# Performance work log

Measured on AMD Instinct MI355X. Metric: run time of the kernel, lower is better.

## Reference

```python
import jax, jax.numpy as jnp
import numpy as np

N_NODES = 50000
N_EDGES = 1_600_000
IN_F, HID, OUT = 256, 256, 64


def setup_inputs() -> dict:
    key = jax.random.key(0)
    ks = jax.random.split(key, 12)
    inp = {
        "x": jax.random.normal(ks[0], (N_NODES, IN_F), dtype=jnp.float32),
        "src": jax.random.randint(ks[1], (N_EDGES,), 0, N_NODES, dtype=jnp.int32),
        "dst": jax.random.randint(ks[2], (N_EDGES,), 0, N_NODES, dtype=jnp.int32),
        "W_self0": jax.random.normal(ks[3], (IN_F, HID), jnp.float32) * (1.0 / np.sqrt(IN_F)),
        "W_neigh0": jax.random.normal(ks[4], (IN_F, HID), jnp.float32) * (1.0 / np.sqrt(IN_F)),
        "b0": jnp.zeros((HID,), jnp.float32),
        "W_self1": jax.random.normal(ks[5], (HID, HID), jnp.float32) * (1.0 / np.sqrt(HID)),
        "W_neigh1": jax.random.normal(ks[6], (HID, HID), jnp.float32) * (1.0 / np.sqrt(HID)),
        "b1": jnp.zeros((HID,), jnp.float32),
        "W_self2": jax.random.normal(ks[7], (HID, OUT), jnp.float32) * (1.0 / np.sqrt(HID)),
        "W_neigh2": jax.random.normal(ks[8], (HID, OUT), jnp.float32) * (1.0 / np.sqrt(HID)),
        "b2": jnp.zeros((OUT,), jnp.float32),
    }
    return inp


def _sage_conv(h, src, dst, W_self, W_neigh, b, n_nodes):
    # mean aggregator: gather source features along edges, segment-mean at dst
    msg = h[src]                                                    # [E, d]
    agg = jax.ops.segment_sum(msg, dst, num_segments=n_nodes)      # [N, d]
    deg = jax.ops.segment_sum(jnp.ones((src.shape[0],), h.dtype), dst,
                              num_segments=n_nodes)                 # [N]
    h_neigh = agg / jnp.maximum(deg, 1.0)[:, None]
    return h @ W_self + h_neigh @ W_neigh + b


def reference(x, src, dst, W_self0, W_neigh0, b0, W_self1, W_neigh1, b1,
              W_self2, W_neigh2, b2):
    n = x.shape[0]
    # dropout is identity at inference
    h = _sage_conv(x, src, dst, W_self0, W_neigh0, b0, n)
    h = jax.nn.relu(h)
    h = _sage_conv(h, src, dst, W_self1, W_neigh1, b1, n)
    h = jax.nn.relu(h)
    last_non_exiting = h
    h = _sage_conv(h, src, dst, W_self2, W_neigh2, b2, n)
    return (h, last_non_exiting)
```

## Files before the change

### kernel.cpp

```cpp
#include <hip/hip_runtime.h>
#include <hip/hip_bf16.h>
#include <cstdint>


typedef __attribute__((ext_vector_type(8))) short  frag_ab;
typedef __attribute__((ext_vector_type(4))) float  f32x4;
typedef __attribute__((ext_vector_type(2))) float  vf2;

#define BIN_T 4096
#define RSHIFT 9
#define RW 512

__device__ __forceinline__ unsigned short f2b(float f) {
    __hip_bfloat16 h = __float2bfloat16(f);
    return *reinterpret_cast<unsigned short*>(&h);
}
__device__ __forceinline__ unsigned char f2p8(float f) {
    int p = __builtin_amdgcn_cvt_pk_fp8_f32(f, f, 0, false);
    return (unsigned char)(p & 0xff);
}
__device__ __forceinline__ void acc8_v(vf2* a, uint4 v) {
    vf2 t0; t0.x = __uint_as_float(v.x << 16); t0.y = __uint_as_float(v.x & 0xffff0000u);
    vf2 t1; t1.x = __uint_as_float(v.y << 16); t1.y = __uint_as_float(v.y & 0xffff0000u);
    vf2 t2; t2.x = __uint_as_float(v.z << 16); t2.y = __uint_as_float(v.z & 0xffff0000u);
    vf2 t3; t3.x = __uint_as_float(v.w << 16); t3.y = __uint_as_float(v.w & 0xffff0000u);
    a[0] += t0; a[1] += t1; a[2] += t2; a[3] += t3;
}
__device__ __forceinline__ void acc16p_v(vf2* a, uint4 v) {
    a[0] += __builtin_amdgcn_cvt_pk_f32_fp8(v.x, false);
    a[1] += __builtin_amdgcn_cvt_pk_f32_fp8(v.x, true);
    a[2] += __builtin_amdgcn_cvt_pk_f32_fp8(v.y, false);
    a[3] += __builtin_amdgcn_cvt_pk_f32_fp8(v.y, true);
    a[4] += __builtin_amdgcn_cvt_pk_f32_fp8(v.z, false);
    a[5] += __builtin_amdgcn_cvt_pk_f32_fp8(v.z, true);
    a[6] += __builtin_amdgcn_cvt_pk_f32_fp8(v.w, false);
    a[7] += __builtin_amdgcn_cvt_pk_f32_fp8(v.w, true);
}

__device__ __forceinline__ void gl_lds16(const void* g, void* l) {
    __builtin_amdgcn_global_load_lds(
        (const __attribute__((address_space(1))) unsigned int*)g,
        (__attribute__((address_space(3))) unsigned int*)l, 16, 0, 0);
}

__global__ __launch_bounds__(512) void bin_edges(
    const int* __restrict__ src, const int* __restrict__ dst,
    int* __restrict__ bdst, int* __restrict__ bsrc,
    int* __restrict__ gcnt, int E, int cap) {
    __shared__ int lds_d[BIN_T];
    __shared__ int lds_s[BIN_T];
    __shared__ unsigned short lds_b[BIN_T];
    __shared__ int hist[8][128];
    __shared__ int cur[8][128];
    __shared__ int tot[128], scn[128], pref[128], gbase[128];

    const int tid = threadIdx.x;
    const int w = tid >> 6;
    const int e0 = blockIdx.x * BIN_T;
    const int base = e0 + tid * 8;

    int d[8], sv[8], bk[8];
    if (e0 + BIN_T <= E) {
        int4 a0 = *reinterpret_cast<const int4*>(dst + base);
        int4 a1 = *reinterpret_cast<const int4*>(dst + base + 4);
        int4 b0 = *reinterpret_cast<const int4*>(src + base);
        int4 b1 = *reinterpret_cast<const int4*>(src + base + 4);
        d[0] = a0.x; d[1] = a0.y; d[2] = a0.z; d[3] = a0.w;
        d[4] = a1.x; d[5] = a1.y; d[6] = a1.z; d[7] = a1.w;
        sv[0] = b0.x; sv[1] = b0.y; sv[2] = b0.z; sv[3] = b0.w;
        sv[4] = b1.x; sv[5] = b1.y; sv[6] = b1.z; sv[7] = b1.w;
#pragma unroll
        for (int j = 0; j < 8; j++) bk[j] = (int)((unsigned)d[j] >> RSHIFT);
    } else {
#pragma unroll
        for (int j = 0; j < 8; j++) {
            int e = base + j;
            if (e < E) {
                d[j] = dst[e]; sv[j] = src[e];
                bk[j] = (int)((unsigned)d[j] >> RSHIFT);
            } else {
                d[j] = 0; sv[j] = 0; bk[j] = -1;
            }
        }
    }

    for (int i = tid; i < 8 * 128; i += 512) ((int*)hist)[i] = 0;
    __syncthreads();
#pragma unroll
    for (int j = 0; j < 8; j++)
        if (bk[j] >= 0) atomicAdd(&hist[w][bk[j]], 1);
    __syncthreads();
    if (tid < 128) {
        int t = 0;
#pragma unroll
        for (int w2 = 0; w2 < 8; w2++) t += hist[w2][tid];
        tot[tid] = t; scn[tid] = t;
    }
    __syncthreads();
#pragma unroll
    for (int off = 1; off < 128; off <<= 1) {
        int v = 0;
        if (tid < 128 && tid >= off) v = scn[tid - off];
        __syncthreads();
        if (tid < 128 && tid >= off) scn[tid] += v;
        __syncthreads();
    }
    if (tid < 128) {
        pref[tid] = scn[tid] - tot[tid];
        gbase[tid] = atomicAdd(&gcnt[tid], tot[tid]);
        int b0 = pref[tid];
#pragma unroll
        for (int w2 = 0; w2 < 8; w2++) { cur[w2][tid] = b0; b0 += hist[w2][tid]; }
    }
    __syncthreads();
#pragma unroll
    for (int j = 0; j < 8; j++) {
        if (bk[j] >= 0) {
            int pos = atomicAdd(&cur[w][bk[j]], 1);
            lds_d[pos] = d[j];
            lds_s[pos] = sv[j];
            lds_b[pos] = (unsigned short)bk[j];
        }
    }
    __syncthreads();
    const int nv = scn[127];
    for (int i = tid; i < nv; i += 512) {
        int b = lds_b[i];
        int off = gbase[b] + (i - pref[b]);
        bdst[(size_t)b * cap + off] = lds_d[i];
        bsrc[(size_t)b * cap + off] = lds_s[i];
    }
}

__global__ __launch_bounds__(256) void hist_deg(
    const int* __restrict__ bdst, const int* __restrict__ gcnt,
    int* __restrict__ deg, int cap, int N) {
    const int b = blockIdx.x;
    const int cnt = gcnt[b];
    __shared__ int h[RW];
    for (int k = threadIdx.x; k < RW; k += 256) h[k] = 0;
    __syncthreads();
    const int* bd = bdst + (size_t)b * cap;
    for (int i = threadIdx.x; i < cnt; i += 256)
        atomicAdd(&h[bd[i] & (RW - 1)], 1);
    __syncthreads();
    const int v0 = b << RSHIFT;
    for (int k = threadIdx.x; k < RW; k += 256) {
        int node = v0 + k;
        if (node < N) deg[node] = h[k];
    }
}

__global__ __launch_bounds__(256) void scatter_direct(
    const int* __restrict__ bdst, const int* __restrict__ bsrc,
    const int* __restrict__ gcnt, const int* __restrict__ row_start,
    int* __restrict__ csr, int cap, int N) {
    const int b = blockIdx.x;
    const int cnt = gcnt[b];
    const int v0 = b << RSHIFT;
    __shared__ int cur[RW];
    for (int k = threadIdx.x; k < RW; k += 256) {
        int node = v0 + k;
        cur[k] = (node < N) ? row_start[node] : 0;
    }
    __syncthreads();
    const int* bd = bdst + (size_t)b * cap;
    const int* bs = bsrc + (size_t)b * cap;
    for (int i = threadIdx.x; i < cnt; i += 256) {
        int dd = bd[i];
        int ss = bs[i];
        int pos = atomicAdd(&cur[dd & (RW - 1)], 1);
        csr[pos] = ss;
    }
}

__global__ __launch_bounds__(256) void scan_partial_kernel(
    const int* __restrict__ deg, int* __restrict__ partials, int n) {
    const int t = threadIdx.x;
    const int i0 = blockIdx.x * 1024 + t * 4;
    int sum = 0;
#pragma unroll
    for (int j = 0; j < 4; j++) { int i = i0 + j; if (i < n) sum += deg[i]; }
#pragma unroll
    for (int off = 32; off; off >>= 1) sum += __shfl_down(sum, off);
    __shared__ int ws[4];
    int lane = t & 63, wid = t >> 6;
    if (lane == 0) ws[wid] = sum;
    __syncthreads();
    if (t == 0) partials[blockIdx.x] = ws[0] + ws[1] + ws[2] + ws[3];
}

__global__ void scan_partials_kernel(int* __restrict__ p, int nb) {
    const int lane = threadIdx.x;
    int carry = 0;
    for (int base = 0; base < nb; base += 64) {
        int i = base + lane;
        int v = (i < nb) ? p[i] : 0;
        int orig = v;
#pragma unroll
        for (int off = 1; off < 64; off <<= 1) {
            int x = __shfl_up(v, off);
            if (lane >= off) v += x;
        }
        int ex = carry + v - orig;
        if (i < nb) p[i] = ex;
        carry += __shfl(v, 63);
    }
}

__global__ __launch_bounds__(256) void scan_final_kernel(
    const int* __restrict__ deg, const int* __restrict__ pscan,
    int* __restrict__ row_start, int n) {
    const int t = threadIdx.x;
    const int i0 = blockIdx.x * 1024 + t * 4;
    int v0 = (i0 + 0 < n) ? deg[i0 + 0] : 0;
    int v1 = (i0 + 1 < n) ? deg[i0 + 1] : 0;
    int v2 = (i0 + 2 < n) ? deg[i0 + 2] : 0;
    int v3 = (i0 + 3 < n) ? deg[i0 + 3] : 0;
    int tot = v0 + v1 + v2 + v3;
    int lane = t & 63, wid = t >> 6;
    int inc = tot;
#pragma unroll
    for (int off = 1; off < 64; off <<= 1) {
        int x = __shfl_up(inc, off);
        if (lane >= off) inc += x;
    }
    __shared__ int wsum[4];
    if (lane == 63) wsum[wid] = inc;
    __syncthreads();
    int wbase = 0;
    for (int w2 = 0; w2 < wid; w2++) wbase += wsum[w2];
    int r = wbase + inc - tot + pscan[blockIdx.x];
    r += v0; if (i0 + 0 < n) row_start[i0 + 1] = r;
    r += v1; if (i0 + 1 < n) row_start[i0 + 2] = r;
    r += v2; if (i0 + 2 < n) row_start[i0 + 3] = r;
    r += v3; if (i0 + 3 < n) row_start[i0 + 4] = r;
    if (blockIdx.x == 0 && t == 0) row_start[0] = 0;
}

__global__ void conv_x_kernel(const float* __restrict__ in, unsigned short* __restrict__ outb,
                              unsigned char* __restrict__ outp,
                              unsigned char* __restrict__ outp2, int n4) {
    int i = blockIdx.x * blockDim.x + threadIdx.x;
    if (blockIdx.x == 0 && threadIdx.x < 64) {
        *reinterpret_cast<unsigned int*>(outp  + (size_t)n4 * 4 + threadIdx.x * 4) = 0u;
        *reinterpret_cast<unsigned int*>(outp2 + (size_t)n4 * 4 + threadIdx.x * 4) = 0u;
    }
    if (i >= n4) return;
    float4 v = *reinterpret_cast<const float4*>(in + (size_t)i * 4);
    ushort4 ob = { f2b(v.x), f2b(v.y), f2b(v.z), f2b(v.w) };
    *reinterpret_cast<ushort4*>(outb + (size_t)i * 4) = ob;
    int p0 = __builtin_amdgcn_cvt_pk_fp8_f32(v.x, v.y, 0, false);
    int p1 = __builtin_amdgcn_cvt_pk_fp8_f32(v.z, v.w, 0, false);
    unsigned int packed = (unsigned int)(p0 & 0xffff) | ((unsigned int)p1 << 16);
    *reinterpret_cast<unsigned int*>(outp + (size_t)i * 4) = packed;
}

__global__ __launch_bounds__(256) void wt_all_kernel(
    const float* __restrict__ Ws0, const float* __restrict__ Wn0,
    const float* __restrict__ Ws1, const float* __restrict__ Wn1,
    const float* __restrict__ Ws2, const float* __restrict__ Wn2,
    unsigned short* __restrict__ Wt0, unsigned short* __restrict__ Wt1,
    unsigned short* __restrict__ Wt2) {
    int b = blockIdx.x;
    const float* W; unsigned short* Wt; int N, koff, Ktot, noff, idx;
    if (b < 1024) {
        int seg = b >> 8; idx = (b & 255) * 256 + threadIdx.x;
        N = 256; Ktot = 512; noff = 0;
        if (seg == 0)      { W = Ws0; Wt = Wt0; koff = 0;   }
        else if (seg == 1) { W = Wn0; Wt = Wt0; koff = 256; }
        else if (seg == 2) { W = Ws1; Wt = Wt1; koff = 0;   }
        else               { W = Wn1; Wt = Wt1; koff = 256; }
    } else {
        int seg = (b - 1024) >> 6; idx = ((b - 1024) & 63) * 256 + threadIdx.x;
        N = 64; Ktot = 256; koff = 0;
        if (seg == 0) { W = Ws2; Wt = Wt2; noff = 0;  }
        else          { W = Wn2; Wt = Wt2; noff = 64; }
    }
    int k = idx / N, n = idx - k * N;
    Wt[(size_t)(n + noff) * Ktot + koff + k] = f2b(W[(size_t)idx]);
}

__global__ __launch_bounds__(256) void agg256_fp8(
    const unsigned char* __restrict__ hsrc, const int* __restrict__ row_start,
    const int* __restrict__ csr, unsigned short* __restrict__ out, int n, int zrow) {
    int wv = (blockIdx.x * blockDim.x + threadIdx.x) >> 6;
    int lane = threadIdx.x & 63;
    if (wv * 4 >= n) return;
    const int q  = lane >> 4;
    const int li = lane & 15;
    const int node = wv * 4 + q;
    const bool act = node < n;
    int s0 = act ? row_start[node] : 0;
    int s1 = act ? row_start[node + 1] : 0;
    int deg = s1 - s0;
    int nmax = deg;
    nmax = max(nmax, __shfl_xor(nmax, 16));
    nmax = max(nmax, __shfl_xor(nmax, 32));

    const size_t lioff = (size_t)li * 16;
    vf2 a[8];
#pragma unroll
    for (int k = 0; k < 8; k++) a[k] = (vf2)(0.f);

#define LD256(vv, k) { int _e = s0 + (k); \
    int _ci = csr[max(min(_e, s1 - 1), 0)]; \
    int _ii = ((k) < deg) ? _ci : zrow; \
    vv = *reinterpret_cast<const uint4*>(hsrc + (size_t)_ii * 256 + lioff); }

    uint4 v0, v1, v2, v3, v4, v5;
    LD256(v0, 0); LD256(v1, 1); LD256(v2, 2);
    LD256(v3, 3); LD256(v4, 4); LD256(v5, 5);
    for (int b = 0; b < nmax; b += 6) {
        acc16p_v(a, v0); LD256(v0, b + 6);
        acc16p_v(a, v1); LD256(v1, b + 7);
        acc16p_v(a, v2); LD256(v2, b + 8);
        acc16p_v(a, v3); LD256(v3, b + 9);
        acc16p_v(a, v4); LD256(v4, b + 10);
        acc16p_v(a, v5); LD256(v5, b + 11);
    }
#undef LD256

    if (act) {
        float sc = 1.0f / (float)max(deg, 1);
        uint4 o0, o1;
        o0.x = ((unsigned)f2b(a[0].y * sc) << 16) | f2b(a[0].x * sc);
        o0.y = ((unsigned)f2b(a[1].y * sc) << 16) | f2b(a[1].x * sc);
        o0.z = ((unsigned)f2b(a[2].y * sc) << 16) | f2b(a[2].x * sc);
        o0.w = ((unsigned)f2b(a[3].y * sc) << 16) | f2b(a[3].x * sc);
        o1.x = ((unsigned)f2b(a[4].y * sc) << 16) | f2b(a[4].x * sc);
        o1.y = ((unsigned)f2b(a[5].y * sc) << 16) | f2b(a[5].x * sc);
        o1.z = ((unsigned)f2b(a[6].y * sc) << 16) | f2b(a[6].x * sc);
        o1.w = ((unsigned)f2b(a[7].y * sc) << 16) | f2b(a[7].x * sc);
        *reinterpret_cast<uint4*>(out + (size_t)node * 256 + li * 16) = o0;
        *reinterpret_cast<uint4*>(out + (size_t)node * 256 + li * 16 + 8) = o1;
    }
}

__global__ __launch_bounds__(256) void agg64_final(
    const unsigned short* __restrict__ t, const int* __restrict__ row_start,
    const int* __restrict__ csr, const float* __restrict__ Sself,
    const float* __restrict__ b2, float* __restrict__ h2, int n) {
    int wv = (blockIdx.x * blockDim.x + threadIdx.x) >> 6;
    int lane = threadIdx.x & 63;
    if (wv * 8 >= n) return;
    const int g  = lane >> 3;
    const int li = lane & 7;
    const int node = wv * 8 + g;
    const bool act = node < n;
    int s0 = act ? row_start[node] : 0;
    int s1 = act ? row_start[node + 1] : 0;
    int deg = s1 - s0;
    int nmax = deg;
    nmax = max(nmax, __shfl_xor(nmax, 8));
    nmax = max(nmax, __shfl_xor(nmax, 16));
    nmax = max(nmax, __shfl_xor(nmax, 32));

    const size_t lioff = (size_t)li * 8;
    vf2 a[4];
#pragma unroll
    for (int k = 0; k < 4; k++) a[k] = (vf2)(0.f);

#define LD64(vv, k) { int _e = s0 + (k); \
    int _ci = csr[max(min(_e, s1 - 1), 0)]; \
    vv = make_uint4(0u, 0u, 0u, 0u); \
    if ((k) < deg) \
        vv = *reinterpret_cast<const uint4*>(t + (size_t)_ci * 64 + lioff); }

    uint4 v0, v1, v2, v3, v4, v5;
    LD64(v0, 0); LD64(v1, 1); LD64(v2, 2);
    LD64(v3, 3); LD64(v4, 4); LD64(v5, 5);
    for (int b = 0; b < nmax; b += 6) {
        acc8_v(a, v0); LD64(v0, b + 6);
        acc8_v(a, v1); LD64(v1, b + 7);
        acc8_v(a, v2); LD64(v2, b + 8);
        acc8_v(a, v3); LD64(v3, b + 9);
        acc8_v(a, v4); LD64(v4, b + 10);
        acc8_v(a, v5); LD64(v5, b + 11);
    }
#undef LD64

    if (act) {
        float sc = 1.0f / (float)max(deg, 1);
        float4 s0v = *reinterpret_cast<const float4*>(Sself + (size_t)node * 64 + li * 8);
        float4 s1v = *reinterpret_cast<const float4*>(Sself + (size_t)node * 64 + li * 8 + 4);
        float4 bb0 = *reinterpret_cast<const float4*>(b2 + li * 8);
        float4 bb1 = *reinterpret_cast<const float4*>(b2 + li * 8 + 4);
        f32x4 o0, o1;
        o0.x = s0v.x + a[0].x * sc + bb0.x; o0.y = s0v.y + a[0].y * sc + bb0.y;
        o0.z = s0v.z + a[1].x * sc + bb0.z; o0.w = s0v.w + a[1].y * sc + bb0.w;
        o1.x = s1v.x + a[2].x * sc + bb1.x; o1.y = s1v.y + a[2].y * sc + bb1.y;
        o1.z = s1v.z + a[3].x * sc + bb1.z; o1.w = s1v.w + a[3].y * sc + bb1.w;
        __builtin_nontemporal_store(o0, reinterpret_cast<f32x4*>(h2 + (size_t)node * 64 + li * 8));
        __builtin_nontemporal_store(o1, reinterpret_cast<f32x4*>(h2 + (size_t)node * 64 + li * 8 + 4));
    }
}

#define BTM 128
#define BTN 256
#define BTK 32

__global__ __launch_bounds__(512, 4) void gemm_big512(
    const unsigned short* __restrict__ A, const unsigned short* __restrict__ G,
    const unsigned short* __restrict__ Wt, const float* __restrict__ bias,
    float* __restrict__ outF, unsigned short* __restrict__ outB,
    unsigned char* __restrict__ outP, int M) {
    __shared__ unsigned short Asb[BTM][BTK];
    __shared__ unsigned short Bsb[BTN][BTK];

    const int tid = threadIdx.x;
    const int row0 = blockIdx.x * BTM;
    const int w = tid >> 6, lane = tid & 63;
    const int mw = (w & 1) * 64;
    const int nw = (w >> 1) * 64;
    const int lm = lane & 15, lq = lane >> 4;
    const int lr = lane >> 2;
    const int lc = (lane & 3) * 8;

    f32x4 acc[4][4];
#pragma unroll
    for (int i = 0; i < 4; i++)
#pragma unroll
        for (int j = 0; j < 4; j++) acc[i][j] = (f32x4)(0.f);

    for (int k0 = 0; k0 < 512; k0 += BTK) {
        const unsigned short* __restrict__ Ap = (k0 >= 256) ? G : A;
        const int kl = k0 & 255;
        {
            int gr = row0 + w * 16 + lr;
            if (gr < M)
                gl_lds16(Ap + (size_t)gr * 256 + kl + lc, &Asb[w * 16][0]);
        }
#pragma unroll
        for (int h = 0; h < 2; ++h) {
            int gn = w * 32 + h * 16 + lr;
            gl_lds16(Wt + (size_t)gn * 512 + k0 + lc, &Bsb[w * 32 + h * 16][0]);
        }
        __syncthreads();

        frag_ab a[4], b[4];
#pragma unroll
        for (int i = 0; i < 4; i++)
            a[i] = *reinterpret_cast<const frag_ab*>(&Asb[mw + i * 16 + lm][lq * 8]);
#pragma unroll
        for (int j = 0; j < 4; j++)
            b[j] = *reinterpret_cast<const frag_ab*>(&Bsb[nw + j * 16 + lm][lq * 8]);
#pragma unroll
        for (int i = 0; i < 4; i++)
#pragma unroll
            for (int j = 0; j < 4; j++)
                acc[i][j] = __builtin_amdgcn_mfma_f32_16x16x32_bf16(a[i], b[j], acc[i][j], 0, 0, 0);
        __syncthreads();
    }

#pragma unroll
    for (int i = 0; i < 4; i++) {
#pragma unroll
        for (int j = 0; j < 4; j++) {
            int cg = nw + j * 16 + lm;
#pragma unroll
            for (int r = 0; r < 4; r++) {
                int rg = row0 + mw + i * 16 + lq * 4 + r;
                if (rg >= M) continue;
                float v = acc[i][j][r] + bias[cg];
                v = fmaxf(v, 0.f);
                outB[(size_t)rg * 256 + cg] = f2b(v);
                if (outF) __builtin_nontemporal_store(v, &outF[(size_t)rg * 256 + cg]);
                if (outP) outP[(size_t)rg * 256 + cg] = f2p8(v);
            }
        }
    }
}

#define TM 128
#define TN 64
#define TK 32

__global__ __launch_bounds__(256) void gemm_mfma(
    const unsigned short* __restrict__ A, const unsigned short* __restrict__ Wt,
    float* __restrict__ outF, unsigned short* __restrict__ outB, int M) {
    __shared__ unsigned short Asb[TM][TK];
    __shared__ unsigned short Bsb[TN][TK];

    const int tid = threadIdx.x;
    const int row0 = blockIdx.x * TM;
    const int col0 = blockIdx.y * TN;

    const int w = tid >> 6, lane = tid & 63;
    const int mw = (w & 1) * 64;
    const int nw = (w >> 1) * 32;
    const int lm = lane & 15, lq = lane >> 4;
    const int lr = lane >> 2;
    const int lc = (lane & 3) * 8;

    f32x4 acc[4][2];
#pragma unroll
    for (int i = 0; i < 4; i++)
#pragma unroll
        for (int j = 0; j < 2; j++) acc[i][j] = (f32x4)(0.f);

    for (int k0 = 0; k0 < 256; k0 += TK) {
#pragma unroll
        for (int h = 0; h < 2; ++h) {
            int r16 = w * 32 + h * 16;
            int gr = row0 + r16 + lr;
            if (gr < M)
                gl_lds16(A + (size_t)gr * 256 + k0 + lc, &Asb[r16][0]);
        }
        {
            int n16 = w * 16;
            int gn = col0 + n16 + lr;
            gl_lds16(Wt + (size_t)gn * 256 + k0 + lc, &Bsb[n16][0]);
        }
        __syncthreads();

        frag_ab a[4], b[2];
#pragma unroll
        for (int i = 0; i < 4; i++)
            a[i] = *reinterpret_cast<const frag_ab*>(&Asb[mw + i * 16 + lm][lq * 8]);
#pragma unroll
        for (int j = 0; j < 2; j++)
            b[j] = *reinterpret_cast<const frag_ab*>(&Bsb[nw + j * 16 + lm][lq * 8]);
#pragma unroll
        for (int i = 0; i < 4; i++)
#pragma unroll
            for (int j = 0; j < 2; j++)
                acc[i][j] = __builtin_amdgcn_mfma_f32_16x16x32_bf16(a[i], b[j], acc[i][j], 0, 0, 0);
        __syncthreads();
    }

#pragma unroll
    for (int i = 0; i < 4; i++) {
#pragma unroll
        for (int j = 0; j < 2; j++) {
            int c = nw + j * 16 + lm;
#pragma unroll
            for (int r = 0; r < 4; r++) {
                int rg = row0 + mw + i * 16 + lq * 4 + r;
                if (rg >= M) continue;
                float v = acc[i][j][r];
                if (col0 == 0) outF[(size_t)rg * 64 + c] = v;
                else           outB[(size_t)rg * 64 + c] = f2b(v);
            }
        }
    }
}

extern "C" void kernel_launch(void* const* d_in, const int* in_sizes, int n_in,
                              void* d_out, int out_size, void* d_ws, size_t ws_size,
                              hipStream_t stream) {
    const float* x   = (const float*)d_in[0];
    const int*   src = (const int*)d_in[1];
    const int*   dst = (const int*)d_in[2];
    const float* Ws0 = (const float*)d_in[3];
    const float* Wn0 = (const float*)d_in[4];
    const float* b0  = (const float*)d_in[5];
    const float* Ws1 = (const float*)d_in[6];
    const float* Wn1 = (const float*)d_in[7];
    const float* b1  = (const float*)d_in[8];
    const float* Ws2 = (const float*)d_in[9];
    const float* Wn2 = (const float*)d_in[10];
    const float* b2  = (const float*)d_in[11];

    const int N = in_sizes[0] / 256;
    const int E = in_sizes[1];

    float* out = (float*)d_out;
    float* h2 = out;
    float* h1 = out + (size_t)N * 64;

    const int nbuk = (N + RW - 1) >> RSHIFT;
    const int cap  = (E + nbuk - 1) / nbuk + 2048;

    char* w = (char*)d_ws;
    auto align16 = [](char* p) { return (char*)(((uintptr_t)p + 15) & ~(uintptr_t)15); };
    int* deg       = (int*)w;  w += (size_t)N * 4;
    int* gcnt      = (int*)w;  w += 128 * 4;
    int* row_start = (int*)w;  w += (size_t)(N + 1) * 4;
    int* partials  = (int*)w;  w += 256 * 4;
    int* csr       = (int*)w;  w += (size_t)E * 4;
    int* bdst      = (int*)w;  w += (size_t)nbuk * cap * 4;
    int* bsrc      = (int*)w;  w += (size_t)nbuk * cap * 4;
    w = align16(w);
    unsigned short* Wt0   = (unsigned short*)w; w += (size_t)256 * 512 * 2;
    unsigned short* Wt1   = (unsigned short*)w; w += (size_t)256 * 512 * 2;
    unsigned short* Wt2   = (unsigned short*)w; w += (size_t)128 * 256 * 2;
    w = align16(w);
    unsigned short* xb    = (unsigned short*)w; w += (size_t)(N + 1) * 256 * 2;
    unsigned short* A1b   = (unsigned short*)w; w += (size_t)N * 256 * 2;
    unsigned short* H0b   = (unsigned short*)w; w += (size_t)(N + 1) * 256 * 2;
    unsigned short* h1b   = (unsigned short*)w; w += (size_t)(N + 1) * 256 * 2;
    unsigned char* x8  = (unsigned char*)H0b;
    unsigned char* H08 = (unsigned char*)h1b;
    unsigned short* Tb    = xb;
    float*          Sself = (float*)A1b;

    const int nb = (N + 1023) / 1024;

    hipMemsetAsync(gcnt, 0, 128 * 4, stream);
    bin_edges<<<(E + BIN_T - 1) / BIN_T, 512, 0, stream>>>(src, dst, bdst, bsrc, gcnt, E, cap);
    hist_deg<<<nbuk, 256, 0, stream>>>(bdst, gcnt, deg, cap, N);
    scan_partial_kernel<<<nb, 256, 0, stream>>>(deg, partials, N);
    scan_partials_kernel<<<1, 64, 0, stream>>>(partials, nb);
    scan_final_kernel<<<nb, 256, 0, stream>>>(deg, partials, row_start, N);
    scatter_direct<<<nbuk, 256, 0, stream>>>(bdst, bsrc, gcnt, row_start, csr, cap, N);

    {
        int n4 = N * 256 / 4;
        conv_x_kernel<<<(n4 + 255) / 256, 256, 0, stream>>>(x, xb, x8, H08, n4);
    }
    wt_all_kernel<<<1152, 256, 0, stream>>>(Ws0, Wn0, Ws1, Wn1, Ws2, Wn2, Wt0, Wt1, Wt2);

    dim3 agg256Grid((N + 15) / 16);
    dim3 agg64Grid((N + 31) / 32);
    dim3 gStripe((N + BTM - 1) / BTM);
    dim3 gL2((N + TM - 1) / TM, 2);

    agg256_fp8<<<agg256Grid, 256, 0, stream>>>(x8, row_start, csr, A1b, N, N);
    gemm_big512<<<gStripe, 512, 0, stream>>>(xb, A1b, Wt0, b0, nullptr, H0b, H08, N);
    agg256_fp8<<<agg256Grid, 256, 0, stream>>>(H08, row_start, csr, A1b, N, N);
    gemm_big512<<<gStripe, 512, 0, stream>>>(H0b, A1b, Wt1, b1, h1, h1b, nullptr, N);
    gemm_mfma<<<gL2, 256, 0, stream>>>(h1b, Wt2, Sself, Tb, N);
    agg64_final<<<agg64Grid, 256, 0, stream>>>(Tb, row_start, csr, Sself, b2, h2, N);
}
```

Before: 444.3 us.

## Double wavefronts in big GEMM and stage epilogue through LDS for vector stores

The stripe GEMM now runs 1024 threads (16 waves), so each wave owns a 64x32 output tile instead of 64x64, which halves per-wave accumulators and spreads the MFMA work across more waves. The epilogue writes accumulators to a shared-memory staging buffer one 16-row slice at a time, then each thread reads 8 contiguous columns, applies bias and ReLU, and issues packed 16-byte bf16, fp32 and 8-byte fp8 stores in place of scattered scalar stores. This targets the poorly coalesced epilogue writes and low occupancy. In exchange it adds extra barriers per slice and larger workgroups, and the launch_bounds value of 8 may not be achievable at this block size.

```diff
diff --git a/kernel.cpp b/kernel.cpp
--- a/kernel.cpp
+++ b/kernel.cpp
@@ -400,73 +400,106 @@
 #define BTN 256
 #define BTK 32
 
-__global__ __launch_bounds__(512, 4) void gemm_big512(
+__global__ __launch_bounds__(1024, 8) void gemm_big512(
     const unsigned short* __restrict__ A, const unsigned short* __restrict__ G,
     const unsigned short* __restrict__ Wt, const float* __restrict__ bias,
     float* __restrict__ outF, unsigned short* __restrict__ outB,
     unsigned char* __restrict__ outP, int M) {
-    __shared__ unsigned short Asb[BTM][BTK];
-    __shared__ unsigned short Bsb[BTN][BTK];
+    __shared__ char smem[32768] __attribute__((aligned(128)));
+    auto Asb = reinterpret_cast<unsigned short(*)[BTK]>(smem);
+    auto Bsb = reinterpret_cast<unsigned short(*)[BTK]>(smem + 8192);
+    float* Cst = reinterpret_cast<float*>(smem);
 
     const int tid = threadIdx.x;
     const int row0 = blockIdx.x * BTM;
     const int w = tid >> 6, lane = tid & 63;
     const int mw = (w & 1) * 64;
-    const int nw = (w >> 1) * 64;
+    const int nw = (w >> 1) * 32;
     const int lm = lane & 15, lq = lane >> 4;
     const int lr = lane >> 2;
     const int lc = (lane & 3) * 8;
 
-    f32x4 acc[4][4];
+    f32x4 acc[4][2];
 #pragma unroll
     for (int i = 0; i < 4; i++)
 #pragma unroll
-        for (int j = 0; j < 4; j++) acc[i][j] = (f32x4)(0.f);
+        for (int j = 0; j < 2; j++) acc[i][j] = (f32x4)(0.f);
 
     for (int k0 = 0; k0 < 512; k0 += BTK) {
         const unsigned short* __restrict__ Ap = (k0 >= 256) ? G : A;
         const int kl = k0 & 255;
-        {
+        if (w < 8) {
             int gr = row0 + w * 16 + lr;
             if (gr < M)
                 gl_lds16(Ap + (size_t)gr * 256 + kl + lc, &Asb[w * 16][0]);
         }
-#pragma unroll
-        for (int h = 0; h < 2; ++h) {
-            int gn = w * 32 + h * 16 + lr;
-            gl_lds16(Wt + (size_t)gn * 512 + k0 + lc, &Bsb[w * 32 + h * 16][0]);
-        }
-        __syncthreads();
-
-        frag_ab a[4], b[4];
+        {
+            int gn = w * 16 + lr;
+            gl_lds16(Wt + (size_t)gn * 512 + k0 + lc, &Bsb[w * 16][0]);
+        }
+        __syncthreads();
+
+        frag_ab a[4], b[2];
 #pragma unroll
         for (int i = 0; i < 4; i++)
             a[i] = *reinterpret_cast<const frag_ab*>(&Asb[mw + i * 16 + lm][lq * 8]);
 #pragma unroll
-        for (int j = 0; j < 4; j++)
+        for (int j = 0; j < 2; j++)
             b[j] = *reinterpret_cast<const frag_ab*>(&Bsb[nw + j * 16 + lm][lq * 8]);
 #pragma unroll
         for (int i = 0; i < 4; i++)
 #pragma unroll
-            for (int j = 0; j < 4; j++)
+            for (int j = 0; j < 2; j++)
                 acc[i][j] = __builtin_amdgcn_mfma_f32_16x16x32_bf16(a[i], b[j], acc[i][j], 0, 0, 0);
         __syncthreads();
     }
 
+    const int r2 = tid >> 5;
+    const int c0 = (tid & 31) * 8;
 #pragma unroll
     for (int i = 0; i < 4; i++) {
-#pragma unroll
-        for (int j = 0; j < 4; j++) {
-            int cg = nw + j * 16 + lm;
-#pragma unroll
-            for (int r = 0; r < 4; r++) {
-                int rg = row0 + mw + i * 16 + lq * 4 + r;
-                if (rg >= M) continue;
-                float v = acc[i][j][r] + bias[cg];
-                v = fmaxf(v, 0.f);
-                outB[(size_t)rg * 256 + cg] = f2b(v);
-                if (outF) __builtin_nontemporal_store(v, &outF[(size_t)rg * 256 + cg]);
-                if (outP) outP[(size_t)rg * 256 + cg] = f2p8(v);
+        __syncthreads();
+        const int lrow = (w & 1) * 16 + lq * 4;
+#pragma unroll
+        for (int j = 0; j < 2; j++) {
+            const int col = nw + j * 16 + lm;
+#pragma unroll
+            for (int r = 0; r < 4; r++)
+                Cst[(lrow + r) * 256 + col] = acc[i][j][r];
+        }
+        __syncthreads();
+        int rg = row0 + (r2 >> 4) * 64 + i * 16 + (r2 & 15);
+        if (rg < M) {
+            float4 v0 = *reinterpret_cast<const float4*>(&Cst[r2 * 256 + c0]);
+            float4 v1 = *reinterpret_cast<const float4*>(&Cst[r2 * 256 + c0 + 4]);
+            float4 bb0 = *reinterpret_cast<const float4*>(bias + c0);
+            float4 bb1 = *reinterpret_cast<const float4*>(bias + c0 + 4);
+            float e0 = fmaxf(v0.x + bb0.x, 0.f), e1 = fmaxf(v0.y + bb0.y, 0.f);
+            float e2 = fmaxf(v0.z + bb0.z, 0.f), e3 = fmaxf(v0.w + bb0.w, 0.f);
+            float e4 = fmaxf(v1.x + bb1.x, 0.f), e5 = fmaxf(v1.y + bb1.y, 0.f);
+            float e6 = fmaxf(v1.z + bb1.z, 0.f), e7 = fmaxf(v1.w + bb1.w, 0.f);
+            uint4 ob;
+            ob.x = ((unsigned)f2b(e1) << 16) | f2b(e0);
+            ob.y = ((unsigned)f2b(e3) << 16) | f2b(e2);
+            ob.z = ((unsigned)f2b(e5) << 16) | f2b(e4);
+            ob.w = ((unsigned)f2b(e7) << 16) | f2b(e6);
+            *reinterpret_cast<uint4*>(outB + (size_t)rg * 256 + c0) = ob;
+            if (outF) {
+                f32x4 f0, f1;
+                f0.x = e0; f0.y = e1; f0.z = e2; f0.w = e3;
+                f1.x = e4; f1.y = e5; f1.z = e6; f1.w = e7;
+                __builtin_nontemporal_store(f0, reinterpret_cast<f32x4*>(outF + (size_t)rg * 256 + c0));
+                __builtin_nontemporal_store(f1, reinterpret_cast<f32x4*>(outF + (size_t)rg * 256 + c0 + 4));
+            }
+            if (outP) {
+                unsigned p01 = (unsigned)__builtin_amdgcn_cvt_pk_fp8_f32(e0, e1, 0, false) & 0xffff;
+                unsigned p23 = (unsigned)__builtin_amdgcn_cvt_pk_fp8_f32(e2, e3, 0, false) & 0xffff;
+                unsigned p45 = (unsigned)__builtin_amdgcn_cvt_pk_fp8_f32(e4, e5, 0, false) & 0xffff;
+                unsigned p67 = (unsigned)__builtin_amdgcn_cvt_pk_fp8_f32(e6, e7, 0, false) & 0xffff;
+                uint2 op;
+                op.x = p01 | (p23 << 16);
+                op.y = p45 | (p67 << 16);
+                *reinterpret_cast<uint2*>(outP + (size_t)rg * 256 + c0) = op;
             }
         }
     }
@@ -617,9 +650,9 @@
     dim3 gL2((N + TM - 1) / TM, 2);
 
     agg256_fp8<<<agg256Grid, 256, 0, stream>>>(x8, row_start, csr, A1b, N, N);
-    gemm_big512<<<gStripe, 512, 0, stream>>>(xb, A1b, Wt0, b0, nullptr, H0b, H08, N);
+    gemm_big512<<<gStripe, 1024, 0, stream>>>(xb, A1b, Wt0, b0, nullptr, H0b, H08, N);
     agg256_fp8<<<agg256Grid, 256, 0, stream>>>(H08, row_start, csr, A1b, N, N);
-    gemm_big512<<<gStripe, 512, 0, stream>>>(H0b, A1b, Wt1, b1, h1, h1b, nullptr, N);
+    gemm_big512<<<gStripe, 1024, 0, stream>>>(H0b, A1b, Wt1, b1, h1, h1b, nullptr, N);
     gemm_mfma<<<gL2, 256, 0, stream>>>(h1b, Wt2, Sself, Tb, N);
     agg64_final<<<agg64Grid, 256, 0, stream>>>(Tb, row_start, csr, Sself, b2, h2, N);
 }
```

After: 452.8 us. Within noise of the previous version (+1.9%).

## Fuse CSR build into bucket-local scan and merge conversion and layer-2 GEMM launches

Applied to the files above, without the earlier changes.

Replaces the degree histogram, three-kernel global scan and scatter with a single-warp scan over bucket counts plus one per-bucket kernel that histograms, scans locally and scatters. The x conversion and weight transpose kernels are merged into one launch, and the layer-2 GEMM computes both 64-column halves in one block, so it runs over a 1-D grid and loads the A tile once. This cuts about five kernel launches and the redundant degree/row_start traffic. In exchange, each CSR block does a serial 512-entry LDS scan with many barriers, and the GEMM uses more accumulator registers.

```diff
diff --git a/kernel.cpp b/kernel.cpp
--- a/kernel.cpp
+++ b/kernel.cpp
@@ -132,39 +132,59 @@
     }
 }
 
-__global__ __launch_bounds__(256) void hist_deg(
-    const int* __restrict__ bdst, const int* __restrict__ gcnt,
-    int* __restrict__ deg, int cap, int N) {
+__global__ void scan_gcnt(const int* __restrict__ gcnt, int* __restrict__ gbase,
+                          int* __restrict__ row_start, int N, int E) {
+    const int lane = threadIdx.x;
+    int v0 = gcnt[lane];
+    int v1 = gcnt[64 + lane];
+    int s0 = v0;
+#pragma unroll
+    for (int off = 1; off < 64; off <<= 1) { int x = __shfl_up(s0, off); if (lane >= off) s0 += x; }
+    int tot0 = __shfl(s0, 63);
+    int s1 = v1;
+#pragma unroll
+    for (int off = 1; off < 64; off <<= 1) { int x = __shfl_up(s1, off); if (lane >= off) s1 += x; }
+    gbase[lane] = s0 - v0;
+    gbase[64 + lane] = tot0 + s1 - v1;
+    if (lane == 0) row_start[N] = E;
+}
+
+__global__ __launch_bounds__(256) void csr_bucket(
+    const int* __restrict__ bdst, const int* __restrict__ bsrc,
+    const int* __restrict__ gcnt, const int* __restrict__ gbase,
+    int* __restrict__ row_start, int* __restrict__ csr, int cap, int N) {
     const int b = blockIdx.x;
     const int cnt = gcnt[b];
+    const int base = gbase[b];
+    const int v0 = b << RSHIFT;
     __shared__ int h[RW];
+    __shared__ int scn[RW];
+    __shared__ int cur[RW];
     for (int k = threadIdx.x; k < RW; k += 256) h[k] = 0;
     __syncthreads();
     const int* bd = bdst + (size_t)b * cap;
     for (int i = threadIdx.x; i < cnt; i += 256)
         atomicAdd(&h[bd[i] & (RW - 1)], 1);
     __syncthreads();
-    const int v0 = b << RSHIFT;
+    for (int k = threadIdx.x; k < RW; k += 256) scn[k] = h[k];
+    __syncthreads();
+    const int k0 = threadIdx.x, k1 = threadIdx.x + 256;
+#pragma unroll
+    for (int off = 1; off < RW; off <<= 1) {
+        int t0 = (k0 >= off) ? scn[k0 - off] : 0;
+        int t1 = (k1 >= off) ? scn[k1 - off] : 0;
+        __syncthreads();
+        scn[k0] += t0;
+        scn[k1] += t1;
+        __syncthreads();
+    }
     for (int k = threadIdx.x; k < RW; k += 256) {
+        int ex = base + scn[k] - h[k];
+        cur[k] = ex;
         int node = v0 + k;
-        if (node < N) deg[node] = h[k];
-    }
-}
-
-__global__ __launch_bounds__(256) void scatter_direct(
-    const int* __restrict__ bdst, const int* __restrict__ bsrc,
-    const int* __restrict__ gcnt, const int* __restrict__ row_start,
-    int* __restrict__ csr, int cap, int N) {
-    const int b = blockIdx.x;
-    const int cnt = gcnt[b];
-    const int v0 = b << RSHIFT;
-    __shared__ int cur[RW];
-    for (int k = threadIdx.x; k < RW; k += 256) {
-        int node = v0 + k;
-        cur[k] = (node < N) ? row_start[node] : 0;
-    }
-    __syncthreads();
-    const int* bd = bdst + (size_t)b * cap;
+        if (node < N) row_start[node] = ex;
+    }
+    __syncthreads();
     const int* bs = bsrc + (size_t)b * cap;
     for (int i = threadIdx.x; i < cnt; i += 256) {
         int dd = bd[i];
@@ -174,110 +194,46 @@
     }
 }
 
-__global__ __launch_bounds__(256) void scan_partial_kernel(
-    const int* __restrict__ deg, int* __restrict__ partials, int n) {
-    const int t = threadIdx.x;
-    const int i0 = blockIdx.x * 1024 + t * 4;
-    int sum = 0;
-#pragma unroll
-    for (int j = 0; j < 4; j++) { int i = i0 + j; if (i < n) sum += deg[i]; }
-#pragma unroll
-    for (int off = 32; off; off >>= 1) sum += __shfl_down(sum, off);
-    __shared__ int ws[4];
-    int lane = t & 63, wid = t >> 6;
-    if (lane == 0) ws[wid] = sum;
-    __syncthreads();
-    if (t == 0) partials[blockIdx.x] = ws[0] + ws[1] + ws[2] + ws[3];
-}
-
-__global__ void scan_partials_kernel(int* __restrict__ p, int nb) {
-    const int lane = threadIdx.x;
-    int carry = 0;
-    for (int base = 0; base < nb; base += 64) {
-        int i = base + lane;
-        int v = (i < nb) ? p[i] : 0;
-        int orig = v;
-#pragma unroll
-        for (int off = 1; off < 64; off <<= 1) {
-            int x = __shfl_up(v, off);
-            if (lane >= off) v += x;
-        }
-        int ex = carry + v - orig;
-        if (i < nb) p[i] = ex;
-        carry += __shfl(v, 63);
-    }
-}
-
-__global__ __launch_bounds__(256) void scan_final_kernel(
-    const int* __restrict__ deg, const int* __restrict__ pscan,
-    int* __restrict__ row_start, int n) {
-    const int t = threadIdx.x;
-    const int i0 = blockIdx.x * 1024 + t * 4;
-    int v0 = (i0 + 0 < n) ? deg[i0 + 0] : 0;
-    int v1 = (i0 + 1 < n) ? deg[i0 + 1] : 0;
-    int v2 = (i0 + 2 < n) ? deg[i0 + 2] : 0;
-    int v3 = (i0 + 3 < n) ? deg[i0 + 3] : 0;
-    int tot = v0 + v1 + v2 + v3;
-    int lane = t & 63, wid = t >> 6;
-    int inc = tot;
-#pragma unroll
-    for (int off = 1; off < 64; off <<= 1) {
-        int x = __shfl_up(inc, off);
-        if (lane >= off) inc += x;
-    }
-    __shared__ int wsum[4];
-    if (lane == 63) wsum[wid] = inc;
-    __syncthreads();
-    int wbase = 0;
-    for (int w2 = 0; w2 < wid; w2++) wbase += wsum[w2];
-    int r = wbase + inc - tot + pscan[blockIdx.x];
-    r += v0; if (i0 + 0 < n) row_start[i0 + 1] = r;
-    r += v1; if (i0 + 1 < n) row_start[i0 + 2] = r;
-    r += v2; if (i0 + 2 < n) row_start[i0 + 3] = r;
-    r += v3; if (i0 + 3 < n) row_start[i0 + 4] = r;
-    if (blockIdx.x == 0 && t == 0) row_start[0] = 0;
-}
-
-__global__ void conv_x_kernel(const float* __restrict__ in, unsigned short* __restrict__ outb,
-                              unsigned char* __restrict__ outp,
-                              unsigned char* __restrict__ outp2, int n4) {
-    int i = blockIdx.x * blockDim.x + threadIdx.x;
-    if (blockIdx.x == 0 && threadIdx.x < 64) {
-        *reinterpret_cast<unsigned int*>(outp  + (size_t)n4 * 4 + threadIdx.x * 4) = 0u;
-        *reinterpret_cast<unsigned int*>(outp2 + (size_t)n4 * 4 + threadIdx.x * 4) = 0u;
-    }
-    if (i >= n4) return;
-    float4 v = *reinterpret_cast<const float4*>(in + (size_t)i * 4);
-    ushort4 ob = { f2b(v.x), f2b(v.y), f2b(v.z), f2b(v.w) };
-    *reinterpret_cast<ushort4*>(outb + (size_t)i * 4) = ob;
-    int p0 = __builtin_amdgcn_cvt_pk_fp8_f32(v.x, v.y, 0, false);
-    int p1 = __builtin_amdgcn_cvt_pk_fp8_f32(v.z, v.w, 0, false);
-    unsigned int packed = (unsigned int)(p0 & 0xffff) | ((unsigned int)p1 << 16);
-    *reinterpret_cast<unsigned int*>(outp + (size_t)i * 4) = packed;
-}
-
-__global__ __launch_bounds__(256) void wt_all_kernel(
+__global__ __launch_bounds__(256) void conv_wt_kernel(
+    const float* __restrict__ in, unsigned short* __restrict__ outb,
+    unsigned char* __restrict__ outp, unsigned char* __restrict__ outp2, int n4, int nConv,
     const float* __restrict__ Ws0, const float* __restrict__ Wn0,
     const float* __restrict__ Ws1, const float* __restrict__ Wn1,
     const float* __restrict__ Ws2, const float* __restrict__ Wn2,
     unsigned short* __restrict__ Wt0, unsigned short* __restrict__ Wt1,
     unsigned short* __restrict__ Wt2) {
-    int b = blockIdx.x;
-    const float* W; unsigned short* Wt; int N, koff, Ktot, noff, idx;
+    if (blockIdx.x < (unsigned)nConv) {
+        int i = blockIdx.x * 256 + threadIdx.x;
+        if (blockIdx.x == 0 && threadIdx.x < 64) {
+            *reinterpret_cast<unsigned int*>(outp  + (size_t)n4 * 4 + threadIdx.x * 4) = 0u;
+            *reinterpret_cast<unsigned int*>(outp2 + (size_t)n4 * 4 + threadIdx.x * 4) = 0u;
+        }
+        if (i >= n4) return;
+        float4 v = *reinterpret_cast<const float4*>(in + (size_t)i * 4);
+        ushort4 ob = { f2b(v.x), f2b(v.y), f2b(v.z), f2b(v.w) };
+        *reinterpret_cast<ushort4*>(outb + (size_t)i * 4) = ob;
+        int p0 = __builtin_amdgcn_cvt_pk_fp8_f32(v.x, v.y, 0, false);
+        int p1 = __builtin_amdgcn_cvt_pk_fp8_f32(v.z, v.w, 0, false);
+        unsigned int packed = (unsigned int)(p0 & 0xffff) | ((unsigned int)p1 << 16);
+        *reinterpret_cast<unsigned int*>(outp + (size_t)i * 4) = packed;
+        return;
+    }
+    int b = blockIdx.x - nConv;
+    const float* W; unsigned short* Wt; int Nn, koff, Ktot, noff, idx;
     if (b < 1024) {
         int seg = b >> 8; idx = (b & 255) * 256 + threadIdx.x;
-        N = 256; Ktot = 512; noff = 0;
+        Nn = 256; Ktot = 512; noff = 0;
         if (seg == 0)      { W = Ws0; Wt = Wt0; koff = 0;   }
         else if (seg == 1) { W = Wn0; Wt = Wt0; koff = 256; }
         else if (seg == 2) { W = Ws1; Wt = Wt1; koff = 0;   }
         else               { W = Wn1; Wt = Wt1; koff = 256; }
     } else {
         int seg = (b - 1024) >> 6; idx = ((b - 1024) & 63) * 256 + threadIdx.x;
-        N = 64; Ktot = 256; koff = 0;
+        Nn = 64; Ktot = 256; koff = 0;
         if (seg == 0) { W = Ws2; Wt = Wt2; noff = 0;  }
         else          { W = Wn2; Wt = Wt2; noff = 64; }
     }
-    int k = idx / N, n = idx - k * N;
+    int k = idx / Nn, n = idx - k * Nn;
     Wt[(size_t)(n + noff) * Ktot + koff + k] = f2b(W[(size_t)idx]);
 }
 
@@ -473,33 +429,29 @@
 }
 
 #define TM 128
-#define TN 64
-#define TK 32
-
-__global__ __launch_bounds__(256) void gemm_mfma(
+
+__global__ __launch_bounds__(256) void gemm_l2(
     const unsigned short* __restrict__ A, const unsigned short* __restrict__ Wt,
     float* __restrict__ outF, unsigned short* __restrict__ outB, int M) {
-    __shared__ unsigned short Asb[TM][TK];
-    __shared__ unsigned short Bsb[TN][TK];
+    __shared__ unsigned short Asb[128][32];
+    __shared__ unsigned short Bsb[128][32];
 
     const int tid = threadIdx.x;
     const int row0 = blockIdx.x * TM;
-    const int col0 = blockIdx.y * TN;
-
     const int w = tid >> 6, lane = tid & 63;
     const int mw = (w & 1) * 64;
-    const int nw = (w >> 1) * 32;
+    const int nw = (w >> 1) * 64;
     const int lm = lane & 15, lq = lane >> 4;
     const int lr = lane >> 2;
     const int lc = (lane & 3) * 8;
 
-    f32x4 acc[4][2];
+    f32x4 acc[4][4];
 #pragma unroll
     for (int i = 0; i < 4; i++)
 #pragma unroll
-        for (int j = 0; j < 2; j++) acc[i][j] = (f32x4)(0.f);
-
-    for (int k0 = 0; k0 < 256; k0 += TK) {
+        for (int j = 0; j < 4; j++) acc[i][j] = (f32x4)(0.f);
+
+    for (int k0 = 0; k0 < 256; k0 += 32) {
 #pragma unroll
         for (int h = 0; h < 2; ++h) {
             int r16 = w * 32 + h * 16;
@@ -507,24 +459,25 @@
             if (gr < M)
                 gl_lds16(A + (size_t)gr * 256 + k0 + lc, &Asb[r16][0]);
         }
-        {
-            int n16 = w * 16;
-            int gn = col0 + n16 + lr;
+#pragma unroll
+        for (int h = 0; h < 2; ++h) {
+            int n16 = w * 32 + h * 16;
+            int gn = n16 + lr;
             gl_lds16(Wt + (size_t)gn * 256 + k0 + lc, &Bsb[n16][0]);
         }
         __syncthreads();
 
-        frag_ab a[4], b[2];
+        frag_ab a[4], b[4];
 #pragma unroll
         for (int i = 0; i < 4; i++)
             a[i] = *reinterpret_cast<const frag_ab*>(&Asb[mw + i * 16 + lm][lq * 8]);
 #pragma unroll
-        for (int j = 0; j < 2; j++)
+        for (int j = 0; j < 4; j++)
             b[j] = *reinterpret_cast<const frag_ab*>(&Bsb[nw + j * 16 + lm][lq * 8]);
 #pragma unroll
         for (int i = 0; i < 4; i++)
 #pragma unroll
-            for (int j = 0; j < 2; j++)
+            for (int j = 0; j < 4; j++)
                 acc[i][j] = __builtin_amdgcn_mfma_f32_16x16x32_bf16(a[i], b[j], acc[i][j], 0, 0, 0);
         __syncthreads();
     }
@@ -532,15 +485,15 @@
 #pragma unroll
     for (int i = 0; i < 4; i++) {
 #pragma unroll
-        for (int j = 0; j < 2; j++) {
-            int c = nw + j * 16 + lm;
+        for (int j = 0; j < 4; j++) {
+            int cg = nw + j * 16 + lm;
 #pragma unroll
             for (int r = 0; r < 4; r++) {
                 int rg = row0 + mw + i * 16 + lq * 4 + r;
                 if (rg >= M) continue;
                 float v = acc[i][j][r];
-                if (col0 == 0) outF[(size_t)rg * 64 + c] = v;
-                else           outB[(size_t)rg * 64 + c] = f2b(v);
+                if (cg < 64) outF[(size_t)rg * 64 + cg] = v;
+                else         outB[(size_t)rg * 64 + (cg - 64)] = f2b(v);
             }
         }
     }
@@ -574,10 +527,9 @@
 
     char* w = (char*)d_ws;
     auto align16 = [](char* p) { return (char*)(((uintptr_t)p + 15) & ~(uintptr_t)15); };
-    int* deg       = (int*)w;  w += (size_t)N * 4;
     int* gcnt      = (int*)w;  w += 128 * 4;
+    int* gbase     = (int*)w;  w += 128 * 4;
     int* row_start = (int*)w;  w += (size_t)(N + 1) * 4;
-    int* partials  = (int*)w;  w += 256 * 4;
     int* csr       = (int*)w;  w += (size_t)E * 4;
     int* bdst      = (int*)w;  w += (size_t)nbuk * cap * 4;
     int* bsrc      = (int*)w;  w += (size_t)nbuk * cap * 4;
@@ -595,31 +547,27 @@
     unsigned short* Tb    = xb;
     float*          Sself = (float*)A1b;
 
-    const int nb = (N + 1023) / 1024;
-
     hipMemsetAsync(gcnt, 0, 128 * 4, stream);
     bin_edges<<<(E + BIN_T - 1) / BIN_T, 512, 0, stream>>>(src, dst, bdst, bsrc, gcnt, E, cap);
-    hist_deg<<<nbuk, 256, 0, stream>>>(bdst, gcnt, deg, cap, N);
-    scan_partial_kernel<<<nb, 256, 0, stream>>>(deg, partials, N);
-    scan_partials_kernel<<<1, 64, 0, stream>>>(partials, nb);
-    scan_final_kernel<<<nb, 256, 0, stream>>>(deg, partials, row_start, N);
-    scatter_direct<<<nbuk, 256, 0, stream>>>(bdst, bsrc, gcnt, row_start, csr, cap, N);
+    scan_gcnt<<<1, 64, 0, stream>>>(gcnt, gbase, row_start, N, E);
+    csr_bucket<<<nbuk, 256, 0, stream>>>(bdst, bsrc, gcnt, gbase, row_start, csr, cap, N);
 
     {
         int n4 = N * 256 / 4;
-        conv_x_kernel<<<(n4 + 255) / 256, 256, 0, stream>>>(x, xb, x8, H08, n4);
-    }
-    wt_all_kernel<<<1152, 256, 0, stream>>>(Ws0, Wn0, Ws1, Wn1, Ws2, Wn2, Wt0, Wt1, Wt2);
+        int nConv = (n4 + 255) / 256;
+        conv_wt_kernel<<<nConv + 1152, 256, 0, stream>>>(
+            x, xb, x8, H08, n4, nConv, Ws0, Wn0, Ws1, Wn1, Ws2, Wn2, Wt0, Wt1, Wt2);
+    }
 
     dim3 agg256Grid((N + 15) / 16);
     dim3 agg64Grid((N + 31) / 32);
     dim3 gStripe((N + BTM - 1) / BTM);
-    dim3 gL2((N + TM - 1) / TM, 2);
+    dim3 gL2((N + TM - 1) / TM);
 
     agg256_fp8<<<agg256Grid, 256, 0, stream>>>(x8, row_start, csr, A1b, N, N);
     gemm_big512<<<gStripe, 512, 0, stream>>>(xb, A1b, Wt0, b0, nullptr, H0b, H08, N);
     agg256_fp8<<<agg256Grid, 256, 0, stream>>>(H08, row_start, csr, A1b, N, N);
     gemm_big512<<<gStripe, 512, 0, stream>>>(H0b, A1b, Wt1, b1, h1, h1b, nullptr, N);
-    gemm_mfma<<<gL2, 256, 0, stream>>>(h1b, Wt2, Sself, Tb, N);
+    gemm_l2<<<gL2, 256, 0, stream>>>(h1b, Wt2, Sself, Tb, N);
     agg64_final<<<agg64Grid, 256, 0, stream>>>(Tb, row_start, csr, Sself, b2, h2, N);
 }
```

Result: slower. 470.3 us (+5.8%).
